# Optimization experiments

Hardware: AMD Instinct MI355X
Metric: run time of the kernel (lower is better)

## Reference

```python
import jax, jax.numpy as jnp
import numpy as np
from jax import lax

SIGMA1, SIGMA2, TRUNCATE = 4.2, 96.0, 4.0


def _gauss_kernel1d(sigma, truncate):
    # scipy-style: radius = int(truncate*sigma + 0.5), normalized Gaussian
    r = int(truncate * sigma + 0.5)
    t = jnp.arange(-r, r + 1, dtype=jnp.float32)
    k = jnp.exp(-0.5 * (t / sigma) ** 2)
    return k / jnp.sum(k)


def _depthwise_conv1d_centered(x_bcl, k):
    # x_bcl: [B, C, L]; k: [K] with K odd. Centered 'same' conv with reflect padding.
    B, C, L = x_bcl.shape
    K = k.shape[0]
    r = (K - 1) // 2
    xp = jnp.pad(x_bcl, ((0, 0), (0, 0), (r, r)), mode='reflect')
    w = jnp.broadcast_to(k[None, None, :], (C, 1, K)).astype(x_bcl.dtype)
    return lax.conv_general_dilated(
        xp, w, window_strides=(1,), padding='VALID',
        feature_group_count=C,
        dimension_numbers=('NCH', 'OIH', 'NCH'))


def setup_inputs() -> dict:
    key = jax.random.key(0)
    x = jax.random.normal(key, (32, 4096, 321), dtype=jnp.float32)  # [B, L, C]
    return {"x": x}


def reference(x) -> jnp.ndarray:
    k1 = _gauss_kernel1d(SIGMA1, TRUNCATE).astype(x.dtype)
    k2 = _gauss_kernel1d(SIGMA2, TRUNCATE).astype(x.dtype)
    x_bcl = jnp.transpose(x, (0, 2, 1))          # [B, C, L]
    y1 = _depthwise_conv1d_centered(x_bcl, k1)   # narrow Gaussian LP
    y2 = _depthwise_conv1d_centered(x_bcl, k2)   # wide Gaussian LP
    seasonal = y1 - y2
    return jnp.transpose(seasonal, (0, 2, 1))    # back to [B, L, C]
```

## Files before the change

### kernel.cpp

```cpp
#include <hip/hip_runtime.h>
#include <math.h>


#define Bdim 32
#define Ldim 4096
#define Cdim 321

#define R1 17
#define K1n 35
#define R2 384
#define K2n 769

#define GA_R 48
#define GA_N 97
#define GB_R 24
#define GB_N 49

#define NG 257
#define NJD 305
#define NGRP_A 20
#define NTJ 33

#define TL 64
#define TROWS 98
#define NLT 64
#define NCT 6
#define NSEG 128

#define GA_OFF 0
#define GB_OFF 128
#define W1_OFF 192
#define K2_OFF 256
#define K2P_OFF 1088
#define E2_OFF 4096
#define D_OFF 4096
#define E_OFF (D_OFF + Bdim*NJD*Cdim)
#define WS_TOT (E_OFF + Bdim*NG*Cdim)

__device__ __forceinline__ int mirror_idx(int a) {
    a = a < 0 ? -a : a;
    a = a > (Ldim - 1) ? 2 * (Ldim - 1) - a : a;
    return a;
}

__device__ __forceinline__ int xcd_swizzle(int bid, int nwg) {
    int q = nwg >> 3, r = nwg & 7;
    int xcd = bid & 7, i = bid >> 3;
    int base = (xcd < r) ? xcd * (q + 1) : r * (q + 1) + (xcd - r) * q;
    return base + i;
}

__device__ __forceinline__ float block_sum_1024(float v, float* partial) {
#pragma unroll
    for (int off = 32; off >= 1; off >>= 1) v += __shfl_down(v, off, 64);
    __syncthreads();
    if ((threadIdx.x & 63) == 0) partial[threadIdx.x >> 6] = v;
    __syncthreads();
    float s = partial[0];
#pragma unroll
    for (int i = 1; i < 16; ++i) s += partial[i];
    return s;
}

__global__ void init_weights_kernel(float* __restrict__ w) {
    __shared__ float partial[16];
    const int tid = threadIdx.x;

    {
        float v = 0.f;
        if (tid < GA_N) { float t = (float)(tid - GA_R) * (1.0f / 12.0f); v = expf(-0.5f * t * t); }
        float s = block_sum_1024(v, partial);
        if (tid < GA_N) w[GA_OFF + tid] = v / s;
    }
    {
        const float sb = sqrtf(96.f * 96.f - 12.f * 12.f) * (1.0f / 16.0f);
        float v = 0.f;
        if (tid < GB_N) { float t = (float)(tid - GB_R) / sb; v = expf(-0.5f * t * t); }
        float s = block_sum_1024(v, partial);
        if (tid < GB_N) w[GB_OFF + tid] = v / s;
    }
    {
        float v = 0.f;
        if (tid < K1n) { float t = (float)(tid - R1) * (1.0f / 4.2f); v = expf(-0.5f * t * t); }
        float s = block_sum_1024(v, partial);
        if (tid < K1n) w[W1_OFF + tid] = v / s;
    }
    {
        float v = 0.f;
        if (tid < K2n) { float t = (float)(tid - R2) * (1.0f / 96.0f); v = expf(-0.5f * t * t); }
        float s = block_sum_1024(v, partial);
        if (tid < K2n) w[K2_OFF + tid] = v / s;
        if (tid < 784) w[K2P_OFF + tid] = (tid < K2n) ? v / s : 0.f;
    }
}

__global__ __launch_bounds__(256) void decimA_kernel(
        const float* __restrict__ x, const float* __restrict__ ga,
        float* __restrict__ d) {
    __shared__ float gs[GA_N];
    if (threadIdx.x < GA_N) gs[threadIdx.x] = ga[threadIdx.x];
    __syncthreads();

    const int lb = xcd_swizzle(blockIdx.x, gridDim.x);
    const int lin = lb * 256 + threadIdx.x;
    const int c = lin % Cdim;
    const int rest = lin / Cdim;
    const int g = rest % NGRP_A;
    const int b = rest / NGRP_A;
    if (b >= Bdim) return;

    const int jj0 = -24 + 16 * g;
    const float* xb = x + b * (Ldim * Cdim) + c;

    float acc[16];
#pragma unroll
    for (int ii = 0; ii < 16; ++ii) acc[ii] = 0.f;

    const bool interior = (jj0 >= 3) && (jj0 <= 237);

#pragma unroll 1
    for (int p = 0; p < 16; ++p) {
        float row[22];
        if (interior) {
            const float* xp = xb + (16 * (jj0 - 3) + p) * Cdim;
#pragma unroll
            for (int i = 0; i < 22; ++i) row[i] = xp[i * (16 * Cdim)];
        } else {
#pragma unroll
            for (int i = 0; i < 22; ++i)
                row[i] = xb[mirror_idx(16 * (jj0 - 3 + i) + p) * Cdim];
        }
#pragma unroll
        for (int q = 0; q < 6; ++q) {
            const float wq = gs[16 * q + p];
#pragma unroll
            for (int ii = 0; ii < 16; ++ii)
                acc[ii] = fmaf(wq, row[ii + q], acc[ii]);
        }
        if (p == 0) {
            const float w6 = gs[96];
#pragma unroll
            for (int ii = 0; ii < 16; ++ii)
                acc[ii] = fmaf(w6, row[ii + 6], acc[ii]);
        }
    }

    const int j0d = jj0 + 24;
    float* db = d + (b * NJD + j0d) * Cdim + c;
#pragma unroll
    for (int ii = 0; ii < 16; ++ii)
        if (j0d + ii < NJD) db[ii * Cdim] = acc[ii];
}

__global__ __launch_bounds__(256) void coarseB_kernel(
        const float* __restrict__ d, const float* __restrict__ gb,
        float* __restrict__ e) {
    __shared__ float gbs[GB_N];
    if (threadIdx.x < GB_N) gbs[threadIdx.x] = gb[threadIdx.x];
    __syncthreads();

    const int lin = blockIdx.x * 256 + threadIdx.x;
    const int c = lin % Cdim;
    const int rest = lin / Cdim;
    const int tj = rest % NTJ;
    const int b = rest / NTJ;
    if (b >= Bdim) return;

    const int j0 = tj * 8;
    const float* db = d + b * (NJD * Cdim) + c;

    float row[56];
#pragma unroll
    for (int r = 0; r < 56; ++r) {
        int idx = j0 + r;
        idx = idx > (NJD - 1) ? (NJD - 1) : idx;
        row[r] = db[idx * Cdim];
    }

    float acc[8];
#pragma unroll
    for (int jj = 0; jj < 8; ++jj) acc[jj] = 0.f;
#pragma unroll
    for (int s = 0; s < GB_N; ++s) {
        const float wv = gbs[s];
#pragma unroll
        for (int jj = 0; jj < 8; ++jj)
            acc[jj] = fmaf(wv, row[s + jj], acc[jj]);
    }

    float* eb = e + (b * NG + j0) * Cdim + c;
#pragma unroll
    for (int jj = 0; jj < 8; ++jj)
        if (j0 + jj < NG) eb[jj * Cdim] = acc[jj];
}

__global__ __launch_bounds__(256, 4) void narrow_lds_kernel(
        const float* __restrict__ x, const float* __restrict__ w1,
        const float* __restrict__ e, float* __restrict__ out) {
    __shared__ float ws[K1n];
    __shared__ float tile[TROWS * 64];
    if (threadIdx.x < K1n) ws[threadIdx.x] = w1[threadIdx.x];

    const int bid = xcd_swizzle(blockIdx.x, gridDim.x);
    const int lt = bid % NLT;
    const int rest = bid / NLT;
    const int ct = rest % NCT;
    const int b = rest / NCT;

    const int c = threadIdx.x & 63;
    const int wv = threadIdx.x >> 6;
    const int c0 = (ct < 5) ? ct * 64 : Cdim - 64;
    const int l0 = lt * TL;
    const float* xb = x + b * (Ldim * Cdim);

    if (lt > 0 && lt < NLT - 1) {
        const float* xp = xb + (l0 - R1) * Cdim + c0 + c;
#pragma unroll
        for (int k = 0; k < 25; ++k) {
            const int r = wv + 4 * k;
            if (r < TROWS) tile[r * 64 + c] = xp[r * Cdim];
        }
    } else {
#pragma unroll
        for (int k = 0; k < 25; ++k) {
            const int r = wv + 4 * k;
            if (r < TROWS) tile[r * 64 + c] = xb[mirror_idx(l0 - R1 + r) * Cdim + c0 + c];
        }
    }
    __syncthreads();

    float row[50];
#pragma unroll
    for (int i = 0; i < 50; ++i) row[i] = tile[(wv * 16 + i) * 64 + c];

    float acc[16];
#pragma unroll
    for (int m = 0; m < 16; ++m) acc[m] = 0.f;
#pragma unroll
    for (int t = 0; t < K1n; ++t) {
        const float wt = ws[t];
#pragma unroll
        for (int m = 0; m < 16; ++m)
            acc[m] = fmaf(wt, row[t + m], acc[m]);
    }

    const int j = (l0 >> 4) + wv;
    const float* eb = e + (b * NG + j) * Cdim + c0 + c;
    const float z0 = eb[0];
    const float z1 = eb[Cdim];
    const float dz = (z1 - z0) * (1.0f / 16.0f);

    float* ob = out + (b * Ldim + l0 + wv * 16) * Cdim + c0 + c;
#pragma unroll
    for (int m = 0; m < 16; ++m)
        ob[m * Cdim] = acc[m] - fmaf(dz, (float)m, z0);
}

__global__ __launch_bounds__(256, 2) void narrow_reg_kernel(
        const float* __restrict__ x, const float* __restrict__ w1,
        const float* __restrict__ e, float* __restrict__ out) {
    __shared__ float ws[K1n];
    if (threadIdx.x < K1n) ws[threadIdx.x] = w1[threadIdx.x];
    __syncthreads();

    const int lb = xcd_swizzle(blockIdx.x, gridDim.x);
    const int lin = lb * 256 + threadIdx.x;
    const int c = lin % Cdim;
    const int rest = lin / Cdim;
    const int seg = rest % NSEG;
    const int b = rest / NSEG;
    if (b >= Bdim) return;

    const int l0 = seg * 32;
    const float* xb = x + b * (Ldim * Cdim) + c;

    const int j0 = seg * 2;
    const float* eb = e + (b * NG + j0) * Cdim + c;
    const float z0 = eb[0];
    const float z1 = eb[Cdim];
    const float z2 = eb[2 * Cdim];

    float row[66];
    if (seg >= 1 && seg <= 126) {
        const float* xp = xb + (l0 - R1) * Cdim;
#pragma unroll
        for (int i = 0; i < 66; ++i) row[i] = xp[i * Cdim];
    } else {
#pragma unroll
        for (int i = 0; i < 66; ++i)
            row[i] = xb[mirror_idx(l0 - R1 + i) * Cdim];
    }

    float acc[32];
#pragma unroll
    for (int m = 0; m < 32; ++m) acc[m] = 0.f;
#pragma unroll
    for (int t = 0; t < K1n; ++t) {
        const float wt = ws[t];
#pragma unroll
        for (int m = 0; m < 32; ++m)
            acc[m] = fmaf(wt, row[t + m], acc[m]);
    }

    const float d0 = (z1 - z0) * (1.0f / 16.0f);
    const float d1 = (z2 - z1) * (1.0f / 16.0f);
    float* ob = out + (b * Ldim + l0) * Cdim + c;
#pragma unroll
    for (int m = 0; m < 16; ++m)
        ob[m * Cdim] = acc[m] - fmaf(d0, (float)m, z0);
#pragma unroll
    for (int m = 16; m < 32; ++m)
        ob[m * Cdim] = acc[m] - fmaf(d1, (float)(m - 16), z1);
}

#define JPT 16
#define NJG 17
__global__ __launch_bounds__(256, 2) void wide_mid_kernel(
        const float* __restrict__ x, const float* __restrict__ w2p,
        float* __restrict__ z) {
    __shared__ float w2s[784];
    for (int i = threadIdx.x; i < 784; i += 256) w2s[i] = w2p[i];
    __syncthreads();

    const int gid = blockIdx.x * 256 + threadIdx.x;
    const int c = gid % Cdim;
    const int rest = gid / Cdim;
    const int jg = rest % NJG;
    const int b = rest / NJG;
    if (b >= Bdim) return;

    const int j0 = jg * JPT;
    const float* xb = x + b * (Ldim * Cdim) + c;

    float acc[JPT];
#pragma unroll
    for (int jj = 0; jj < JPT; ++jj) acc[jj] = 0.f;

    const bool interior = (j0 >= 24) && (16 * (j0 + 39) + 15 <= Ldim - 1);

#pragma unroll 1
    for (int p = 0; p < 16; ++p) {
        float row[64];
        if (interior) {
            const float* xp = xb + (16 * (j0 - 24) + p) * Cdim;
#pragma unroll
            for (int i = 0; i < 64; ++i) row[i] = xp[i * (16 * Cdim)];
        } else {
#pragma unroll
            for (int i = 0; i < 64; ++i)
                row[i] = xb[mirror_idx(16 * (j0 - 24 + i) + p) * Cdim];
        }
#pragma unroll
        for (int q = 0; q < 49; ++q) {
            const float wq = w2s[q * 16 + p];
#pragma unroll
            for (int jj = 0; jj < JPT; ++jj)
                acc[jj] = fmaf(wq, row[q + jj], acc[jj]);
        }
    }

    float* zb = z + (b * NG + j0) * Cdim + c;
#pragma unroll
    for (int jj = 0; jj < JPT; ++jj)
        if (j0 + jj < NG) zb[jj * Cdim] = acc[jj];
}

__global__ __launch_bounds__(256) void naive_kernel(
        const float* __restrict__ x, const float* __restrict__ w,
        float* __restrict__ out) {
    const int gid = blockIdx.x * 256 + threadIdx.x;
    if (gid >= Bdim * Ldim * Cdim) return;
    const int c = gid % Cdim;
    const int rest = gid / Cdim;
    const int l = rest % Ldim;
    const int b = rest / Ldim;
    const float* xb = x + b * (Ldim * Cdim) + c;
    float a2 = 0.f, a1 = 0.f;
    for (int t = 0; t < K2n; ++t)
        a2 = fmaf(w[K2_OFF + t], xb[mirror_idx(l + t - R2) * Cdim], a2);
#pragma unroll
    for (int t = 0; t < K1n; ++t)
        a1 = fmaf(w[W1_OFF + t], xb[mirror_idx(l + t - R1) * Cdim], a1);
    out[gid] = a1 - a2;
}

extern "C" void kernel_launch(void* const* d_in, const int* in_sizes, int n_in,
                              void* d_out, int out_size, void* d_ws, size_t ws_size,
                              hipStream_t stream) {
    (void)in_sizes; (void)n_in; (void)out_size;
    const float* x = (const float*)d_in[0];
    float* out = (float*)d_out;
    float* w = (float*)d_ws;

    hipLaunchKernelGGL(init_weights_kernel, dim3(1), dim3(1024), 0, stream, w);

    const size_t need_pyr = (size_t)WS_TOT * sizeof(float);
    const size_t need_mid = (size_t)(E2_OFF + Bdim * NG * Cdim) * sizeof(float);

    if (ws_size >= need_pyr) {
        const int a_total = Bdim * NGRP_A * Cdim;
        hipLaunchKernelGGL(decimA_kernel, dim3((a_total + 255) / 256), dim3(256),
                           0, stream, x, w + GA_OFF, w + D_OFF);
        const int b_total = Bdim * NTJ * Cdim;
        hipLaunchKernelGGL(coarseB_kernel, dim3((b_total + 255) / 256), dim3(256),
                           0, stream, w + D_OFF, w + GB_OFF, w + E_OFF);
        const int nblk = Bdim * NCT * NLT;
        hipLaunchKernelGGL(narrow_lds_kernel, dim3(nblk), dim3(256),
                           0, stream, x, w + W1_OFF, w + E_OFF, out);
    } else if (ws_size >= need_mid) {
        const int wide_total = Bdim * NJG * Cdim;
        hipLaunchKernelGGL(wide_mid_kernel, dim3((wide_total + 255) / 256), dim3(256),
                           0, stream, x, w + K2P_OFF, w + E2_OFF);
        const int nar_total = Bdim * NSEG * Cdim;
        hipLaunchKernelGGL(narrow_reg_kernel, dim3((nar_total + 255) / 256), dim3(256),
                           0, stream, x, w + W1_OFF, w + E2_OFF, out);
    } else {
        const int total = Bdim * Ldim * Cdim;
        hipLaunchKernelGGL(naive_kernel, dim3((total + 255) / 256), dim3(256),
                           0, stream, x, w, out);
    }
}
```

Measured before the change: 170.6 us.

## Stream narrow-conv input through an LDS ring with async global-to-LDS loads

The narrow Gaussian stage now has each block walk a 256-row strip through a 128-row LDS ring buffer. Rows are staged with global_load_lds direct copies and the next 32-row chunk is prefetched while the current one is computed, so the 34-row halo is no longer reloaded for every 64-row tile. Threads compute two channels at once with packed float2 FMAs, and the leftover 321st channel moves to a separate small kernel instead of overlapping column tiles. In exchange each block has a longer serial loop with a barrier per chunk, and there is one extra kernel launch.

```diff
diff --git a/kernel.cpp b/kernel.cpp
--- a/kernel.cpp
+++ b/kernel.cpp
@@ -21,10 +21,12 @@
 #define NGRP_A 20
 #define NTJ 33
 
-#define TL 64
-#define TROWS 98
-#define NLT 64
-#define NCT 6
+#define LBLK11 256
+#define NLB11 16
+#define NCT11 5
+#define RING 128
+#define RSTR 64
+#define NSUB 8
 #define NSEG 128
 
 #define GA_OFF 0
@@ -37,6 +39,8 @@
 #define E_OFF (D_OFF + Bdim*NJD*Cdim)
 #define WS_TOT (E_OFF + Bdim*NG*Cdim)
 
+typedef float f32x2 __attribute__((ext_vector_type(2)));
+
 __device__ __forceinline__ int mirror_idx(int a) {
     a = a < 0 ? -a : a;
     a = a > (Ldim - 1) ? 2 * (Ldim - 1) - a : a;
@@ -194,44 +198,117 @@
         if (j0 + jj < NG) eb[jj * Cdim] = acc[jj];
 }
 
-__global__ __launch_bounds__(256, 4) void narrow_lds_kernel(
+__global__ __launch_bounds__(256) void narrow_v11_kernel(
         const float* __restrict__ x, const float* __restrict__ w1,
         const float* __restrict__ e, float* __restrict__ out) {
     __shared__ float ws[K1n];
-    __shared__ float tile[TROWS * 64];
+    __shared__ float tile[RING * RSTR];
     if (threadIdx.x < K1n) ws[threadIdx.x] = w1[threadIdx.x];
 
     const int bid = xcd_swizzle(blockIdx.x, gridDim.x);
-    const int lt = bid % NLT;
-    const int rest = bid / NLT;
-    const int ct = rest % NCT;
-    const int b = rest / NCT;
-
-    const int c = threadIdx.x & 63;
+    const int ct = bid % NCT11;
+    const int rest = bid / NCT11;
+    const int lb = rest % NLB11;
+    const int b = rest / NLB11;
+
+    const int c0 = ct * 64;
+    const int L0 = lb * LBLK11;
+    const int lane = threadIdx.x & 63;
     const int wv = threadIdx.x >> 6;
-    const int c0 = (ct < 5) ? ct * 64 : Cdim - 64;
-    const int l0 = lt * TL;
-    const float* xb = x + b * (Ldim * Cdim);
-
-    if (lt > 0 && lt < NLT - 1) {
-        const float* xp = xb + (l0 - R1) * Cdim + c0 + c;
-#pragma unroll
-        for (int k = 0; k < 25; ++k) {
-            const int r = wv + 4 * k;
-            if (r < TROWS) tile[r * 64 + c] = xp[r * Cdim];
-        }
+    const float* xb = x + (size_t)b * (Ldim * Cdim);
+
+    auto STAGE = [&](int r0, int nrows) {
+#pragma unroll 1
+        for (int k = 0;; ++k) {
+            const int p = wv + 4 * k;
+            if (4 * p >= nrows) break;
+            const int rlog = r0 + 4 * p + (lane >> 4);
+            const int srow = mirror_idx(rlog);
+            const float* g = xb + (size_t)srow * Cdim + c0 + (lane & 15) * 4;
+            const int slot = (r0 + 4 * p) & (RING - 1);
+            __builtin_amdgcn_global_load_lds(
+                (const __attribute__((address_space(1))) void*)g,
+                (__attribute__((address_space(3))) void*)(&tile[slot * RSTR]),
+                16, 0, 0);
+        }
+    };
+
+    STAGE(L0 - 20, 72);
+    __syncthreads();
+
+    const int cp = threadIdx.x & 31;
+    const int lgrp = threadIdx.x >> 5;
+    const int c2 = c0 + 2 * cp;
+    const int fbase = (4 * lgrp) & 15;
+
+#pragma unroll 1
+    for (int s = 0; s < NSUB; ++s) {
+        const int l0s = L0 + 32 * s;
+        if (s + 1 < NSUB) STAGE(l0s + 52, 32);
+
+        const int rbase = l0s + 4 * lgrp - R1;
+        f32x2 r2[38];
+#pragma unroll
+        for (int i = 0; i < 38; ++i)
+            r2[i] = *reinterpret_cast<const f32x2*>(
+                &tile[((rbase + i) & (RING - 1)) * RSTR + 2 * cp]);
+
+        f32x2 acc[4];
+#pragma unroll
+        for (int m = 0; m < 4; ++m) acc[m] = (f32x2)(0.f);
+#pragma unroll
+        for (int t = 0; t < K1n; ++t) {
+            const float wt = ws[t];
+            const f32x2 w2 = {wt, wt};
+#pragma unroll
+            for (int m = 0; m < 4; ++m)
+                acc[m] = __builtin_elementwise_fma(w2, r2[t + m], acc[m]);
+        }
+
+        const int j = (l0s >> 4) + (lgrp >> 2);
+        const float* eb = e + ((size_t)b * NG + j) * Cdim + c2;
+        const float z0x = eb[0],    z0y = eb[1];
+        const float z1x = eb[Cdim], z1y = eb[Cdim + 1];
+        const float dzx = (z1x - z0x) * 0.0625f;
+        const float dzy = (z1y - z0y) * 0.0625f;
+
+        float* ob = out + ((size_t)b * Ldim + l0s + 4 * lgrp) * Cdim + c2;
+#pragma unroll
+        for (int m = 0; m < 4; ++m) {
+            const float fm = (float)(fbase + m);
+            ob[m * Cdim]     = acc[m].x - fmaf(dzx, fm, z0x);
+            ob[m * Cdim + 1] = acc[m].y - fmaf(dzy, fm, z0y);
+        }
+
+        __syncthreads();
+    }
+}
+
+__global__ __launch_bounds__(256) void narrow_c320_kernel(
+        const float* __restrict__ x, const float* __restrict__ w1,
+        const float* __restrict__ e, float* __restrict__ out) {
+    __shared__ float ws[K1n];
+    if (threadIdx.x < K1n) ws[threadIdx.x] = w1[threadIdx.x];
+    __syncthreads();
+
+    const int gid = blockIdx.x * 256 + threadIdx.x;
+    const int seg = gid & 255;
+    const int b = gid >> 8;
+    if (b >= Bdim) return;
+
+    const int l0 = seg * 16;
+    const float* xc = x + (size_t)b * (Ldim * Cdim) + 320;
+
+    float row[50];
+    if (seg >= 2 && seg <= 253) {
+        const float* p = xc + (size_t)(l0 - R1) * Cdim;
+#pragma unroll
+        for (int i = 0; i < 50; ++i) row[i] = p[(size_t)i * Cdim];
     } else {
 #pragma unroll
-        for (int k = 0; k < 25; ++k) {
-            const int r = wv + 4 * k;
-            if (r < TROWS) tile[r * 64 + c] = xb[mirror_idx(l0 - R1 + r) * Cdim + c0 + c];
-        }
-    }
-    __syncthreads();
-
-    float row[50];
-#pragma unroll
-    for (int i = 0; i < 50; ++i) row[i] = tile[(wv * 16 + i) * 64 + c];
+        for (int i = 0; i < 50; ++i)
+            row[i] = xc[(size_t)mirror_idx(l0 - R1 + i) * Cdim];
+    }
 
     float acc[16];
 #pragma unroll
@@ -244,13 +321,12 @@
             acc[m] = fmaf(wt, row[t + m], acc[m]);
     }
 
-    const int j = (l0 >> 4) + wv;
-    const float* eb = e + (b * NG + j) * Cdim + c0 + c;
-    const float z0 = eb[0];
-    const float z1 = eb[Cdim];
-    const float dz = (z1 - z0) * (1.0f / 16.0f);
-
-    float* ob = out + (b * Ldim + l0 + wv * 16) * Cdim + c0 + c;
+    const int j = l0 >> 4;
+    const float z0 = e[((size_t)b * NG + j) * Cdim + 320];
+    const float z1 = e[((size_t)b * NG + j + 1) * Cdim + 320];
+    const float dz = (z1 - z0) * 0.0625f;
+
+    float* ob = out + ((size_t)b * Ldim + l0) * Cdim + 320;
 #pragma unroll
     for (int m = 0; m < 16; ++m)
         ob[m * Cdim] = acc[m] - fmaf(dz, (float)m, z0);
@@ -404,8 +480,10 @@
         const int b_total = Bdim * NTJ * Cdim;
         hipLaunchKernelGGL(coarseB_kernel, dim3((b_total + 255) / 256), dim3(256),
                            0, stream, w + D_OFF, w + GB_OFF, w + E_OFF);
-        const int nblk = Bdim * NCT * NLT;
-        hipLaunchKernelGGL(narrow_lds_kernel, dim3(nblk), dim3(256),
+        const int nblk = Bdim * NLB11 * NCT11;
+        hipLaunchKernelGGL(narrow_v11_kernel, dim3(nblk), dim3(256),
+                           0, stream, x, w + W1_OFF, w + E_OFF, out);
+        hipLaunchKernelGGL(narrow_c320_kernel, dim3(Bdim), dim3(256),
                            0, stream, x, w + W1_OFF, w + E_OFF, out);
     } else if (ws_size >= need_mid) {
         const int wide_total = Bdim * NJG * Cdim;
```

Result: slower. 183.8 us (+7.7%).
